# Optimization experiments

Measured on AMD Instinct MI355X. Metric: run time of the kernel, lower is better.

The kernel has to match this reference:

```python
import jax, jax.numpy as jnp
import numpy as np

TEMPERATURE = 8.0


def setup_inputs() -> dict:
    key = jax.random.key(0)
    kq, kk, kv, km = jax.random.split(key, 4)
    B, H, S, D = 2, 16, 2048, 64
    q = jax.random.normal(kq, (B, H, S, D), dtype=jnp.float32)
    k = jax.random.normal(kk, (B, H, S, D), dtype=jnp.float32)
    v = jax.random.normal(kv, (B, H, S, D), dtype=jnp.float32)
    mask = jax.random.randint(km, (B, S, S), 0, 2, dtype=jnp.int32)
    return {"q": q, "k": k, "v": v, "mask": mask}


def reference(q, k, v, mask):
    # attn = q @ k^T / temperature  -> [B,H,Sq,Sk]
    attn = jnp.einsum("bhqd,bhkd->bhqk", q, k) / TEMPERATURE
    # mask: [B,Sq,Sk] -> [B,1,Sq,Sk]; masked where mask == 0
    m0 = (mask == 0)[:, None, :, :]
    attn = jnp.where(m0, -jnp.inf, attn)
    attn = jax.nn.softmax(attn, axis=-1)
    attn = jnp.where(m0, 0.0, attn)
    output = jnp.einsum("bhqk,bhkd->bhqd", attn, v)
    return (output, attn)
```

## Files before the change

### kernel.cpp

```cpp
#include <hip/hip_runtime.h>


#define S 2048
#define D 64
#define HH 16
#define BB 2
#define LDK 72

typedef __attribute__((ext_vector_type(8))) short short8;
typedef __attribute__((ext_vector_type(8))) unsigned short ushort8;
typedef __attribute__((ext_vector_type(4))) float f32x4;

__device__ __forceinline__ unsigned short f2bf(float f) {
  unsigned int u = __builtin_bit_cast(unsigned int, f);
  u += 0x7fffu + ((u >> 16) & 1u);
  return (unsigned short)(u >> 16);
}

__device__ __forceinline__ ushort8 cvt8(float4 a, float4 b) {
  ushort8 r;
  r[0] = f2bf(a.x); r[1] = f2bf(a.y); r[2] = f2bf(a.z); r[3] = f2bf(a.w);
  r[4] = f2bf(b.x); r[5] = f2bf(b.y); r[6] = f2bf(b.z); r[7] = f2bf(b.w);
  return r;
}

__global__ __launch_bounds__(256) void attn_kernel(
    const float* __restrict__ Qg, const float* __restrict__ Kg,
    const float* __restrict__ Vg, const int* __restrict__ Mg,
    float* __restrict__ Og, float* __restrict__ Ag) {
  __shared__ unsigned short Kt[64 * LDK];
  __shared__ unsigned short Vt[64 * LDK];
  __shared__ unsigned short Qs[64 * LDK];

  const int tid = threadIdx.x;
  const int w = tid >> 6;
  const int lane = tid & 63;
  const int ln15 = lane & 15;
  const int quad = lane >> 4;

  const int qtile = blockIdx.x;
  const int bh = blockIdx.y;
  const int b = bh >> 4;

  const size_t qkvbase = (size_t)bh * S * D;
  const int q0 = qtile * 64;

  {
    const int trow = tid >> 2;
    const int tcol = (tid & 3) << 4;
    const float4* src =
        reinterpret_cast<const float4*>(Qg + qkvbase + (size_t)(q0 + trow) * D + tcol);
    float4 x0 = src[0], x1 = src[1], x2 = src[2], x3 = src[3];
    *reinterpret_cast<ushort8*>(&Qs[trow * LDK + tcol]) = cvt8(x0, x1);
    *reinterpret_cast<ushort8*>(&Qs[trow * LDK + tcol + 8]) = cvt8(x2, x3);
  }
  __syncthreads();
  const short8 aq0 = *reinterpret_cast<const short8*>(&Qs[(w * 16 + ln15) * LDK + (quad << 3)]);
  const short8 aq1 = *reinterpret_cast<const short8*>(&Qs[(w * 16 + ln15) * LDK + 32 + (quad << 3)]);

  const int qbase = q0 + w * 16 + quad * 4;
  const int* maskrow[4];
#pragma unroll
  for (int r = 0; r < 4; r++)
    maskrow[r] = Mg + (size_t)b * S * S + (size_t)(qbase + r) * S;

  float lsum[4] = {0.f, 0.f, 0.f, 0.f};
  for (int k0 = 0; k0 < S; k0 += 64) {
    __syncthreads();
    {
      const int trow = tid >> 2;
      const int tcol = (tid & 3) << 4;
      const float4* src =
          reinterpret_cast<const float4*>(Kg + qkvbase + (size_t)(k0 + trow) * D + tcol);
      float4 x0 = src[0], x1 = src[1], x2 = src[2], x3 = src[3];
      *reinterpret_cast<ushort8*>(&Kt[trow * LDK + tcol]) = cvt8(x0, x1);
      *reinterpret_cast<ushort8*>(&Kt[trow * LDK + tcol + 8]) = cvt8(x2, x3);
    }
    __syncthreads();
#pragma unroll
    for (int kt = 0; kt < 4; kt++) {
      f32x4 acc = {0.f, 0.f, 0.f, 0.f};
      short8 bk0 = *reinterpret_cast<const short8*>(&Kt[(kt * 16 + ln15) * LDK + (quad << 3)]);
      short8 bk1 = *reinterpret_cast<const short8*>(&Kt[(kt * 16 + ln15) * LDK + 32 + (quad << 3)]);
      acc = __builtin_amdgcn_mfma_f32_16x16x32_bf16(aq0, bk0, acc, 0, 0, 0);
      acc = __builtin_amdgcn_mfma_f32_16x16x32_bf16(aq1, bk1, acc, 0, 0, 0);
      const int key = k0 + kt * 16 + ln15;
#pragma unroll
      for (int r = 0; r < 4; r++) {
        int mv = maskrow[r][key];
        float e = __expf(acc[r] * 0.125f);
        lsum[r] += mv ? e : 0.f;
      }
    }
  }
#pragma unroll
  for (int r = 0; r < 4; r++) {
    float v = lsum[r];
    v += __shfl_xor(v, 1, 64);
    v += __shfl_xor(v, 2, 64);
    v += __shfl_xor(v, 4, 64);
    v += __shfl_xor(v, 8, 64);
    lsum[r] = (v > 0.f) ? 1.f / v : 0.f;
  }

  float* attnrow[4];
#pragma unroll
  for (int r = 0; r < 4; r++)
    attnrow[r] = Ag + ((size_t)bh * S + (size_t)(qbase + r)) * S;

  f32x4 oacc[4] = {{0.f, 0.f, 0.f, 0.f}, {0.f, 0.f, 0.f, 0.f},
                   {0.f, 0.f, 0.f, 0.f}, {0.f, 0.f, 0.f, 0.f}};
  unsigned short* Ps = Qs;

  for (int k0 = 0; k0 < S; k0 += 64) {
    __syncthreads();
    {
      const int trow = tid >> 2;
      const int tcol = (tid & 3) << 4;
      const float4* src =
          reinterpret_cast<const float4*>(Kg + qkvbase + (size_t)(k0 + trow) * D + tcol);
      float4 x0 = src[0], x1 = src[1], x2 = src[2], x3 = src[3];
      *reinterpret_cast<ushort8*>(&Kt[trow * LDK + tcol]) = cvt8(x0, x1);
      *reinterpret_cast<ushort8*>(&Kt[trow * LDK + tcol + 8]) = cvt8(x2, x3);
      const float4* vsrc =
          reinterpret_cast<const float4*>(Vg + qkvbase + (size_t)(k0 + trow) * D + tcol);
      float4 y0 = vsrc[0], y1 = vsrc[1], y2 = vsrc[2], y3 = vsrc[3];
      float yy[16] = {y0.x, y0.y, y0.z, y0.w, y1.x, y1.y, y1.z, y1.w,
                      y2.x, y2.y, y2.z, y2.w, y3.x, y3.y, y3.z, y3.w};
#pragma unroll
      for (int j = 0; j < 16; j++) Vt[(tcol + j) * LDK + trow] = f2bf(yy[j]);
    }
    __syncthreads();
#pragma unroll
    for (int kt = 0; kt < 4; kt++) {
      f32x4 acc = {0.f, 0.f, 0.f, 0.f};
      short8 bk0 = *reinterpret_cast<const short8*>(&Kt[(kt * 16 + ln15) * LDK + (quad << 3)]);
      short8 bk1 = *reinterpret_cast<const short8*>(&Kt[(kt * 16 + ln15) * LDK + 32 + (quad << 3)]);
      acc = __builtin_amdgcn_mfma_f32_16x16x32_bf16(aq0, bk0, acc, 0, 0, 0);
      acc = __builtin_amdgcn_mfma_f32_16x16x32_bf16(aq1, bk1, acc, 0, 0, 0);
      const int key = k0 + kt * 16 + ln15;
#pragma unroll
      for (int r = 0; r < 4; r++) {
        int mv = maskrow[r][key];
        float e = __expf(acc[r] * 0.125f);
        e = mv ? e : 0.f;
        float p = e * lsum[r];
        attnrow[r][key] = p;
        Ps[(w * 16 + quad * 4 + r) * LDK + kt * 16 + ln15] = f2bf(p);
      }
    }
#pragma unroll
    for (int kc = 0; kc < 2; kc++) {
      short8 ap =
          *reinterpret_cast<const short8*>(&Ps[(w * 16 + ln15) * LDK + kc * 32 + (quad << 3)]);
#pragma unroll
      for (int c = 0; c < 4; c++) {
        short8 bv =
            *reinterpret_cast<const short8*>(&Vt[(c * 16 + ln15) * LDK + kc * 32 + (quad << 3)]);
        oacc[c] = __builtin_amdgcn_mfma_f32_16x16x32_bf16(ap, bv, oacc[c], 0, 0, 0);
      }
    }
  }

#pragma unroll
  for (int c = 0; c < 4; c++) {
#pragma unroll
    for (int r = 0; r < 4; r++) {
      Og[qkvbase + (size_t)(qbase + r) * D + c * 16 + ln15] = oacc[c][r];
    }
  }
}

extern "C" void kernel_launch(void* const* d_in, const int* in_sizes, int n_in,
                              void* d_out, int out_size, void* d_ws, size_t ws_size,
                              hipStream_t stream) {
  const float* q = (const float*)d_in[0];
  const float* k = (const float*)d_in[1];
  const float* v = (const float*)d_in[2];
  const int* m = (const int*)d_in[3];
  float* outp = (float*)d_out;
  float* attnp = outp + (size_t)BB * HH * S * D;
  dim3 grid(S / 64, BB * HH);
  attn_kernel<<<grid, 256, 0, stream>>>(q, k, v, m, outp, attnp);
}
```

Measured before the change: 958.6 us.

## Pack mask to bitmask, transpose MFMA operands, vectorize attn stores, prefetch K/V

A pre-pass kernel packs the int32 mask into 64-bit ballot words in workspace, so the attention kernel reads one word per 64 keys instead of an int per element across 16 heads. The QK MFMA operands are swapped so each lane owns a query row and four consecutive keys, which allows float4 stores of the attention matrix and a single lane-local row sum. Q is loaded straight to registers, K/V tiles are register-prefetched one iteration ahead, and the V transpose in LDS uses an XOR swizzle to cut bank conflicts. P moves to a per-wave packed buffer. The cost is an extra kernel launch and workspace use, and the grid order changes to iterate heads fastest, which improves mask reuse in cache.

```diff
diff --git a/kernel.cpp b/kernel.cpp
--- a/kernel.cpp
+++ b/kernel.cpp
@@ -6,31 +6,42 @@
 #define HH 16
 #define BB 2
 #define LDK 72
+#define PSTR 36
 
 typedef __attribute__((ext_vector_type(8))) short short8;
-typedef __attribute__((ext_vector_type(8))) unsigned short ushort8;
 typedef __attribute__((ext_vector_type(4))) float f32x4;
 
-__device__ __forceinline__ unsigned short f2bf(float f) {
+__device__ __forceinline__ unsigned int f2bfu(float f) {
   unsigned int u = __builtin_bit_cast(unsigned int, f);
   u += 0x7fffu + ((u >> 16) & 1u);
-  return (unsigned short)(u >> 16);
-}
-
-__device__ __forceinline__ ushort8 cvt8(float4 a, float4 b) {
-  ushort8 r;
-  r[0] = f2bf(a.x); r[1] = f2bf(a.y); r[2] = f2bf(a.z); r[3] = f2bf(a.w);
-  r[4] = f2bf(b.x); r[5] = f2bf(b.y); r[6] = f2bf(b.z); r[7] = f2bf(b.w);
-  return r;
+  return u >> 16;
+}
+__device__ __forceinline__ unsigned int packbf2(float a, float b) {
+  return f2bfu(a) | (f2bfu(b) << 16);
+}
+__device__ __forceinline__ short8 cvt8(float4 a, float4 b) {
+  union { unsigned int u[4]; short8 s; } r;
+  r.u[0] = packbf2(a.x, a.y); r.u[1] = packbf2(a.z, a.w);
+  r.u[2] = packbf2(b.x, b.y); r.u[3] = packbf2(b.z, b.w);
+  return r.s;
+}
+
+__global__ __launch_bounds__(256) void pack_mask_kernel(
+    const int* __restrict__ m, unsigned long long* __restrict__ bits) {
+  int wid = blockIdx.x * 4 + (threadIdx.x >> 6);
+  int lane = threadIdx.x & 63;
+  int v = m[(size_t)wid * 64 + lane];
+  unsigned long long b = __ballot(v != 0);
+  if (lane == 0) bits[wid] = b;
 }
 
 __global__ __launch_bounds__(256) void attn_kernel(
     const float* __restrict__ Qg, const float* __restrict__ Kg,
-    const float* __restrict__ Vg, const int* __restrict__ Mg,
+    const float* __restrict__ Vg, const unsigned long long* __restrict__ Mb,
     float* __restrict__ Og, float* __restrict__ Ag) {
   __shared__ unsigned short Kt[64 * LDK];
   __shared__ unsigned short Vt[64 * LDK];
-  __shared__ unsigned short Qs[64 * LDK];
+  __shared__ unsigned int Pp[4 * 16 * PSTR];
 
   const int tid = threadIdx.x;
   const int w = tid >> 6;
@@ -38,135 +49,140 @@
   const int ln15 = lane & 15;
   const int quad = lane >> 4;
 
-  const int qtile = blockIdx.x;
-  const int bh = blockIdx.y;
+  const int bh = blockIdx.x;
+  const int qtile = blockIdx.y;
   const int b = bh >> 4;
-
   const size_t qkvbase = (size_t)bh * S * D;
   const int q0 = qtile * 64;
-
+  const int qrow = q0 + w * 16 + ln15;
+
+  const float4* qp = reinterpret_cast<const float4*>(Qg + qkvbase + (size_t)qrow * D);
+  short8 aq0, aq1;
   {
-    const int trow = tid >> 2;
-    const int tcol = (tid & 3) << 4;
-    const float4* src =
-        reinterpret_cast<const float4*>(Qg + qkvbase + (size_t)(q0 + trow) * D + tcol);
-    float4 x0 = src[0], x1 = src[1], x2 = src[2], x3 = src[3];
-    *reinterpret_cast<ushort8*>(&Qs[trow * LDK + tcol]) = cvt8(x0, x1);
-    *reinterpret_cast<ushort8*>(&Qs[trow * LDK + tcol + 8]) = cvt8(x2, x3);
-  }
-  __syncthreads();
-  const short8 aq0 = *reinterpret_cast<const short8*>(&Qs[(w * 16 + ln15) * LDK + (quad << 3)]);
-  const short8 aq1 = *reinterpret_cast<const short8*>(&Qs[(w * 16 + ln15) * LDK + 32 + (quad << 3)]);
-
-  const int qbase = q0 + w * 16 + quad * 4;
-  const int* maskrow[4];
-#pragma unroll
-  for (int r = 0; r < 4; r++)
-    maskrow[r] = Mg + (size_t)b * S * S + (size_t)(qbase + r) * S;
-
-  float lsum[4] = {0.f, 0.f, 0.f, 0.f};
-  for (int k0 = 0; k0 < S; k0 += 64) {
-    __syncthreads();
-    {
-      const int trow = tid >> 2;
-      const int tcol = (tid & 3) << 4;
-      const float4* src =
-          reinterpret_cast<const float4*>(Kg + qkvbase + (size_t)(k0 + trow) * D + tcol);
-      float4 x0 = src[0], x1 = src[1], x2 = src[2], x3 = src[3];
-      *reinterpret_cast<ushort8*>(&Kt[trow * LDK + tcol]) = cvt8(x0, x1);
-      *reinterpret_cast<ushort8*>(&Kt[trow * LDK + tcol + 8]) = cvt8(x2, x3);
-    }
-    __syncthreads();
-#pragma unroll
-    for (int kt = 0; kt < 4; kt++) {
-      f32x4 acc = {0.f, 0.f, 0.f, 0.f};
+    float4 a0 = qp[quad * 2], a1 = qp[quad * 2 + 1];
+    float4 b0 = qp[8 + quad * 2], b1 = qp[8 + quad * 2 + 1];
+    aq0 = cvt8(a0, a1);
+    aq1 = cvt8(b0, b1);
+  }
+
+  const unsigned long long* mrow = Mb + ((size_t)b * S + qrow) * (S / 64);
+
+  const int trow = tid >> 2;
+  const int tcol = (tid & 3) << 4;
+
+  float lsum = 0.f;
+  float4 kf0, kf1, kf2, kf3;
+  {
+    const float4* src = reinterpret_cast<const float4*>(Kg + qkvbase + (size_t)trow * D + tcol);
+    kf0 = src[0]; kf1 = src[1]; kf2 = src[2]; kf3 = src[3];
+  }
+  unsigned long long mw = mrow[0];
+  for (int t = 0; t < 32; ++t) {
+    __syncthreads();
+    *reinterpret_cast<short8*>(&Kt[trow * LDK + tcol]) = cvt8(kf0, kf1);
+    *reinterpret_cast<short8*>(&Kt[trow * LDK + tcol + 8]) = cvt8(kf2, kf3);
+    __syncthreads();
+    if (t < 31) {
+      const float4* src = reinterpret_cast<const float4*>(
+          Kg + qkvbase + (size_t)((t + 1) * 64 + trow) * D + tcol);
+      kf0 = src[0]; kf1 = src[1]; kf2 = src[2]; kf3 = src[3];
+    }
+    unsigned long long mwn = (t < 31) ? mrow[t + 1] : 0ULL;
+#pragma unroll
+    for (int kt = 0; kt < 4; ++kt) {
       short8 bk0 = *reinterpret_cast<const short8*>(&Kt[(kt * 16 + ln15) * LDK + (quad << 3)]);
       short8 bk1 = *reinterpret_cast<const short8*>(&Kt[(kt * 16 + ln15) * LDK + 32 + (quad << 3)]);
-      acc = __builtin_amdgcn_mfma_f32_16x16x32_bf16(aq0, bk0, acc, 0, 0, 0);
-      acc = __builtin_amdgcn_mfma_f32_16x16x32_bf16(aq1, bk1, acc, 0, 0, 0);
-      const int key = k0 + kt * 16 + ln15;
-#pragma unroll
-      for (int r = 0; r < 4; r++) {
-        int mv = maskrow[r][key];
+      f32x4 acc = {0.f, 0.f, 0.f, 0.f};
+      acc = __builtin_amdgcn_mfma_f32_16x16x32_bf16(bk0, aq0, acc, 0, 0, 0);
+      acc = __builtin_amdgcn_mfma_f32_16x16x32_bf16(bk1, aq1, acc, 0, 0, 0);
+      unsigned int nib = (unsigned int)(mw >> (kt * 16 + quad * 4)) & 0xFu;
+#pragma unroll
+      for (int r = 0; r < 4; ++r) {
         float e = __expf(acc[r] * 0.125f);
-        lsum[r] += mv ? e : 0.f;
-      }
-    }
-  }
-#pragma unroll
-  for (int r = 0; r < 4; r++) {
-    float v = lsum[r];
-    v += __shfl_xor(v, 1, 64);
-    v += __shfl_xor(v, 2, 64);
-    v += __shfl_xor(v, 4, 64);
-    v += __shfl_xor(v, 8, 64);
-    lsum[r] = (v > 0.f) ? 1.f / v : 0.f;
-  }
-
-  float* attnrow[4];
-#pragma unroll
-  for (int r = 0; r < 4; r++)
-    attnrow[r] = Ag + ((size_t)bh * S + (size_t)(qbase + r)) * S;
-
+        lsum += ((nib >> r) & 1u) ? e : 0.f;
+      }
+    }
+    mw = mwn;
+  }
+  lsum += __shfl_xor(lsum, 16, 64);
+  lsum += __shfl_xor(lsum, 32, 64);
+  const float rinv = (lsum > 0.f) ? 1.f / lsum : 0.f;
+
+  float* arow = Ag + ((size_t)bh * S + qrow) * S;
   f32x4 oacc[4] = {{0.f, 0.f, 0.f, 0.f}, {0.f, 0.f, 0.f, 0.f},
                    {0.f, 0.f, 0.f, 0.f}, {0.f, 0.f, 0.f, 0.f}};
-  unsigned short* Ps = Qs;
-
-  for (int k0 = 0; k0 < S; k0 += 64) {
-    __syncthreads();
+  unsigned int* Pw = Pp + w * 16 * PSTR;
+
+  float4 vf0, vf1, vf2, vf3;
+  {
+    const float4* src = reinterpret_cast<const float4*>(Kg + qkvbase + (size_t)trow * D + tcol);
+    kf0 = src[0]; kf1 = src[1]; kf2 = src[2]; kf3 = src[3];
+    const float4* vs = reinterpret_cast<const float4*>(Vg + qkvbase + (size_t)trow * D + tcol);
+    vf0 = vs[0]; vf1 = vs[1]; vf2 = vs[2]; vf3 = vs[3];
+  }
+  mw = mrow[0];
+  for (int t = 0; t < 32; ++t) {
+    __syncthreads();
+    *reinterpret_cast<short8*>(&Kt[trow * LDK + tcol]) = cvt8(kf0, kf1);
+    *reinterpret_cast<short8*>(&Kt[trow * LDK + tcol + 8]) = cvt8(kf2, kf3);
     {
-      const int trow = tid >> 2;
-      const int tcol = (tid & 3) << 4;
-      const float4* src =
-          reinterpret_cast<const float4*>(Kg + qkvbase + (size_t)(k0 + trow) * D + tcol);
-      float4 x0 = src[0], x1 = src[1], x2 = src[2], x3 = src[3];
-      *reinterpret_cast<ushort8*>(&Kt[trow * LDK + tcol]) = cvt8(x0, x1);
-      *reinterpret_cast<ushort8*>(&Kt[trow * LDK + tcol + 8]) = cvt8(x2, x3);
-      const float4* vsrc =
-          reinterpret_cast<const float4*>(Vg + qkvbase + (size_t)(k0 + trow) * D + tcol);
-      float4 y0 = vsrc[0], y1 = vsrc[1], y2 = vsrc[2], y3 = vsrc[3];
-      float yy[16] = {y0.x, y0.y, y0.z, y0.w, y1.x, y1.y, y1.z, y1.w,
-                      y2.x, y2.y, y2.z, y2.w, y3.x, y3.y, y3.z, y3.w};
-#pragma unroll
-      for (int j = 0; j < 16; j++) Vt[(tcol + j) * LDK + trow] = f2bf(yy[j]);
-    }
-    __syncthreads();
-#pragma unroll
-    for (int kt = 0; kt < 4; kt++) {
-      f32x4 acc = {0.f, 0.f, 0.f, 0.f};
+      float yy[16] = {vf0.x, vf0.y, vf0.z, vf0.w, vf1.x, vf1.y, vf1.z, vf1.w,
+                      vf2.x, vf2.y, vf2.z, vf2.w, vf3.x, vf3.y, vf3.z, vf3.w};
+#pragma unroll
+      for (int j = 0; j < 16; ++j) {
+        int d = tcol + j;
+        int pg = (trow >> 3) ^ ((d >> 3) & 7);
+        Vt[d * LDK + pg * 8 + (trow & 7)] = (unsigned short)f2bfu(yy[j]);
+      }
+    }
+    __syncthreads();
+    if (t < 31) {
+      const float4* src = reinterpret_cast<const float4*>(
+          Kg + qkvbase + (size_t)((t + 1) * 64 + trow) * D + tcol);
+      kf0 = src[0]; kf1 = src[1]; kf2 = src[2]; kf3 = src[3];
+      const float4* vs = reinterpret_cast<const float4*>(
+          Vg + qkvbase + (size_t)((t + 1) * 64 + trow) * D + tcol);
+      vf0 = vs[0]; vf1 = vs[1]; vf2 = vs[2]; vf3 = vs[3];
+    }
+    unsigned long long mwn = (t < 31) ? mrow[t + 1] : 0ULL;
+    const int k0 = t * 64;
+#pragma unroll
+    for (int kt = 0; kt < 4; ++kt) {
       short8 bk0 = *reinterpret_cast<const short8*>(&Kt[(kt * 16 + ln15) * LDK + (quad << 3)]);
       short8 bk1 = *reinterpret_cast<const short8*>(&Kt[(kt * 16 + ln15) * LDK + 32 + (quad << 3)]);
-      acc = __builtin_amdgcn_mfma_f32_16x16x32_bf16(aq0, bk0, acc, 0, 0, 0);
-      acc = __builtin_amdgcn_mfma_f32_16x16x32_bf16(aq1, bk1, acc, 0, 0, 0);
-      const int key = k0 + kt * 16 + ln15;
-#pragma unroll
-      for (int r = 0; r < 4; r++) {
-        int mv = maskrow[r][key];
-        float e = __expf(acc[r] * 0.125f);
-        e = mv ? e : 0.f;
-        float p = e * lsum[r];
-        attnrow[r][key] = p;
-        Ps[(w * 16 + quad * 4 + r) * LDK + kt * 16 + ln15] = f2bf(p);
-      }
-    }
-#pragma unroll
-    for (int kc = 0; kc < 2; kc++) {
-      short8 ap =
-          *reinterpret_cast<const short8*>(&Ps[(w * 16 + ln15) * LDK + kc * 32 + (quad << 3)]);
-#pragma unroll
-      for (int c = 0; c < 4; c++) {
-        short8 bv =
-            *reinterpret_cast<const short8*>(&Vt[(c * 16 + ln15) * LDK + kc * 32 + (quad << 3)]);
+      f32x4 acc = {0.f, 0.f, 0.f, 0.f};
+      acc = __builtin_amdgcn_mfma_f32_16x16x32_bf16(bk0, aq0, acc, 0, 0, 0);
+      acc = __builtin_amdgcn_mfma_f32_16x16x32_bf16(bk1, aq1, acc, 0, 0, 0);
+      unsigned int nib = (unsigned int)(mw >> (kt * 16 + quad * 4)) & 0xFu;
+      f32x4 p;
+#pragma unroll
+      for (int r = 0; r < 4; ++r) {
+        float e = __expf(acc[r] * 0.125f) * rinv;
+        p[r] = ((nib >> r) & 1u) ? e : 0.f;
+      }
+      *reinterpret_cast<f32x4*>(arow + k0 + kt * 16 + quad * 4) = p;
+      Pw[ln15 * PSTR + kt * 8 + quad * 2] = packbf2(p[0], p[1]);
+      Pw[ln15 * PSTR + kt * 8 + quad * 2 + 1] = packbf2(p[2], p[3]);
+    }
+#pragma unroll
+    for (int kc = 0; kc < 2; ++kc) {
+      short8 ap = *reinterpret_cast<const short8*>(&Pw[ln15 * PSTR + kc * 16 + quad * 4]);
+#pragma unroll
+      for (int c = 0; c < 4; ++c) {
+        int dr = c * 16 + ln15;
+        int pg = (4 * kc + quad) ^ ((dr >> 3) & 7);
+        short8 bv = *reinterpret_cast<const short8*>(&Vt[dr * LDK + pg * 8]);
         oacc[c] = __builtin_amdgcn_mfma_f32_16x16x32_bf16(ap, bv, oacc[c], 0, 0, 0);
       }
     }
-  }
-
-#pragma unroll
-  for (int c = 0; c < 4; c++) {
-#pragma unroll
-    for (int r = 0; r < 4; r++) {
-      Og[qkvbase + (size_t)(qbase + r) * D + c * 16 + ln15] = oacc[c][r];
+    mw = mwn;
+  }
+
+#pragma unroll
+  for (int c = 0; c < 4; ++c) {
+#pragma unroll
+    for (int r = 0; r < 4; ++r) {
+      Og[qkvbase + (size_t)(q0 + w * 16 + quad * 4 + r) * D + c * 16 + ln15] = oacc[c][r];
     }
   }
 }
@@ -180,6 +196,10 @@
   const int* m = (const int*)d_in[3];
   float* outp = (float*)d_out;
   float* attnp = outp + (size_t)BB * HH * S * D;
-  dim3 grid(S / 64, BB * HH);
-  attn_kernel<<<grid, 256, 0, stream>>>(q, k, v, m, outp, attnp);
-}
+  unsigned long long* bits = (unsigned long long*)d_ws;
+
+  const int nwords = BB * S * (S / 64);
+  pack_mask_kernel<<<nwords / 4, 256, 0, stream>>>(m, bits);
+  dim3 grid(BB * HH, S / 64);
+  attn_kernel<<<grid, 256, 0, stream>>>(q, k, v, bits, outp, attnp);
+}
```

After: 804.5 us. -16.1%, faster.
